# Optimization experiments

Hardware: AMD Instinct MI355X
Metric: run time of the kernel (lower is better)

## Reference

```python
import jax, jax.numpy as jnp
import numpy as np
import math

# BDH config (defaults from BDHConfig)
D = 256        # n_embd
NH = 4         # n_head
MULT = 128     # mlp_internal_dim_multiplier
N = MULT * D // NH   # 8192 latent dim per head
NLAYER = 6
VOCAB = 256
B, T = 1, 1024
THETA = 2.0 ** 16
TWO_PI = 2.0 * math.pi


def _freqs(n):
    # get_freqs: quantize exponent to even integers
    t = jnp.arange(n, dtype=jnp.float32)
    q = jnp.floor(t / 2.0) * 2.0
    return 1.0 / (THETA ** (q / n)) / TWO_PI  # [N]


def _ln(x, eps=1e-5):
    # LayerNorm without affine params (elementwise_affine=False)
    m = jnp.mean(x, axis=-1, keepdims=True)
    v = jnp.mean((x - m) ** 2, axis=-1, keepdims=True)
    return (x - m) / jnp.sqrt(v + eps)


def _rope(phases, v):
    # phases: [T,N] broadcastable to v [...,T,N]
    ph = (phases % 1.0) * TWO_PI
    cos, sin = jnp.cos(ph), jnp.sin(ph)
    # rotate adjacent pairs: (-v_odd, v_even) interleaved
    vrot = jnp.stack((-v[..., 1::2], v[..., ::2]), axis=-1).reshape(v.shape)
    return v * cos + vrot * sin


def setup_inputs() -> dict:
    key = jax.random.key(0)
    ks = jax.random.split(key, 6)
    std = 0.02
    return {
        "idx": jax.random.randint(ks[0], (B, T), 0, VOCAB),
        "embed_w": jax.random.normal(ks[1], (VOCAB, D), jnp.float32) * std,
        "encoder": jax.random.normal(ks[2], (NH, D, N), jnp.float32) * std,
        "encoder_v": jax.random.normal(ks[3], (NH, D, N), jnp.float32) * std,
        "decoder": jax.random.normal(ks[4], (NH * N, D), jnp.float32) * std,
        "lm_head": jax.random.normal(ks[5], (D, VOCAB), jnp.float32) * std,
    }


def reference(idx, embed_w, encoder, encoder_v, decoder, lm_head):
    freqs = _freqs(N)                                             # [N]
    phases = jnp.arange(T, dtype=jnp.float32)[:, None] * freqs    # [T,N]
    mask = jnp.tril(jnp.ones((T, T), jnp.float32), k=-1)          # strict causal
    dec = decoder.reshape(NH, N, D)

    x = _ln(embed_w[idx])                                         # [B,T,D]
    for _ in range(NLAYER):
        x_sp = jax.nn.relu(jnp.einsum('btd,hdn->bhtn', x, encoder))   # [B,nh,T,N]
        qr = _rope(phases, x_sp)                                       # [B,nh,T,N]
        scores = jnp.einsum('bhtn,bhsn->bhts', qr, qr) * mask          # [B,nh,T,T]
        ykv = _ln(jnp.einsum('bhts,bsd->bhtd', scores, x))             # [B,nh,T,D]
        y_sp = jax.nn.relu(jnp.einsum('bhtd,hdn->bhtn', ykv, encoder_v))
        xy = x_sp * y_sp                                               # [B,nh,T,N]
        ymlp = jnp.einsum('bhtn,hnd->btd', xy, dec)                    # [B,T,D]
        x = _ln(x + _ln(ymlp))
    return x @ lm_head                                                 # [B,T,VOCAB]
```

## Files before the change

kernel.cpp:

```cpp
#include <hip/hip_runtime.h>
#include <hip/hip_bf16.h>
#include <math.h>

#define T_ 1024
#define D_ 256
#define N_ 8192
#define NH_ 4
#define NLAYER_ 6
#define VOCAB_ 256
#define TWO_PI_F 6.283185307179586f
#define INV_TWO_PI_F 0.15915494309189535f

#define SC_HSTR32 294912u
#define SC_SSTR32 1179648u
#define SC_SPLIT_BYTES 4718592u
#define SC_NSPLIT 8

typedef __attribute__((ext_vector_type(8))) short short8;
typedef __attribute__((ext_vector_type(4))) float floatx4;
typedef unsigned short ushort_t;

__device__ __forceinline__ void cp16(const void* g, void* l) {
    __builtin_amdgcn_global_load_lds((const __attribute__((address_space(1))) unsigned int*)g,
                                     (__attribute__((address_space(3))) unsigned int*)l,
                                     16, 0, 0);
}

__device__ __forceinline__ float bf2f_raw(unsigned short u) {
    union { unsigned int i; float f; } x;
    x.i = ((unsigned int)u) << 16;
    return x.f;
}
__device__ __forceinline__ unsigned int f2bf_u(float f) {
    union { float f; unsigned int u; } x; x.f = f;
    return (x.u + 0x7fffu + ((x.u >> 16) & 1u)) >> 16;
}

__device__ __forceinline__ float block_sum(float v, float* red) {
    int tid = threadIdx.x;
    red[tid] = v;
    __syncthreads();
    #pragma unroll
    for (int s = 128; s > 0; s >>= 1) {
        if (tid < s) red[tid] += red[tid + s];
        __syncthreads();
    }
    float r = red[0];
    __syncthreads();
    return r;
}


__global__ void k_embed_ln(const int* __restrict__ idx, const float* __restrict__ ew,
                           float* __restrict__ x, __hip_bfloat16* __restrict__ x_bf) {
    __shared__ float red[256];
    int t = blockIdx.x, d = threadIdx.x;
    float v = ew[idx[t] * D_ + d];
    float mean = block_sum(v, red) * (1.0f / D_);
    float c = v - mean;
    float var = block_sum(c * c, red) * (1.0f / D_);
    float o = c * rsqrtf(var + 1e-5f);
    x[t * D_ + d] = o;
    x_bf[t * D_ + d] = __float2bfloat16(o);
}

__global__ void k_ln_rows(const float* __restrict__ yp, __hip_bfloat16* __restrict__ outb) {
    __shared__ float red[256];
    int r = blockIdx.x, d = threadIdx.x;
    const size_t S = (size_t)NH_ * T_ * D_;
    float v = yp[(size_t)r * D_ + d] + yp[S + (size_t)r * D_ + d];
    float mean = block_sum(v, red) * (1.0f / D_);
    float c = v - mean;
    float var = block_sum(c * c, red) * (1.0f / D_);
    outb[(size_t)r * D_ + d] = __float2bfloat16(c * rsqrtf(var + 1e-5f));
}

__global__ void k_x_update(float* __restrict__ x, const float* __restrict__ ypart,
                           __hip_bfloat16* __restrict__ x_bf) {
    __shared__ float red[256];
    int t = blockIdx.x, d = threadIdx.x;
    float v = 0.0f;
    #pragma unroll
    for (int i = 0; i < 32; i++) v += ypart[(size_t)i * T_ * D_ + t * D_ + d];
    float m1 = block_sum(v, red) * (1.0f / D_);
    float c1 = v - m1;
    float v1 = block_sum(c1 * c1, red) * (1.0f / D_);
    float u = c1 * rsqrtf(v1 + 1e-5f);
    float w = x[t * D_ + d] + u;
    float m2 = block_sum(w, red) * (1.0f / D_);
    float c2 = w - m2;
    float v2 = block_sum(c2 * c2, red) * (1.0f / D_);
    float o = c2 * rsqrtf(v2 + 1e-5f);
    x[t * D_ + d] = o;
    x_bf[t * D_ + d] = __float2bfloat16(o);
}

__global__ __launch_bounds__(256) void k_tcvt(const float* __restrict__ in,
                                              __hip_bfloat16* __restrict__ out,
                                              int R, int C) {
    int h = blockIdx.z;
    int r0 = blockIdx.y * 32, c0 = blockIdx.x * 32;
    __shared__ float tile[32][33];
    int tx = threadIdx.x & 31, ty = threadIdx.x >> 5;
    const float* inh = in + (size_t)h * R * C;
    __hip_bfloat16* outh = out + (size_t)h * R * C;
    #pragma unroll
    for (int i = 0; i < 4; i++)
        tile[ty + 8 * i][tx] = inh[(size_t)(r0 + ty + 8 * i) * C + c0 + tx];
    __syncthreads();
    #pragma unroll
    for (int i = 0; i < 4; i++)
        outh[(size_t)(c0 + ty + 8 * i) * R + r0 + tx] = __float2bfloat16(tile[tx][ty + 8 * i]);
}

__device__ __forceinline__ void gemm128(const ushort_t* __restrict__ A,
                                        const ushort_t* __restrict__ B,
                                        int lda, int ldb, int K,
                                        ushort_t* As, ushort_t* Bs,
                                        floatx4 acc[4][4]) {
    const int tid = threadIdx.x;
    const int lane = tid & 63, wid = tid >> 6;
    const int wm = wid >> 1, wn = wid & 1;
    const int quad = lane >> 4, col = lane & 15;
    int srow[4], scol[4];
    #pragma unroll
    for (int i = 0; i < 4; i++) {
        int s = i * 256 + tid;
        srow[i] = s >> 3;
        scol[i] = (s & 7) ^ (srow[i] & 7);
    }
    for (int k0 = 0; k0 < K; k0 += 64) {
        #pragma unroll
        for (int i = 0; i < 4; i++)
            cp16(A + (size_t)srow[i] * lda + k0 + scol[i] * 8,
                 As + (size_t)(i * 256 + wid * 64) * 8);
        #pragma unroll
        for (int i = 0; i < 4; i++)
            cp16(B + (size_t)srow[i] * ldb + k0 + scol[i] * 8,
                 Bs + (size_t)(i * 256 + wid * 64) * 8);
        __syncthreads();
        #pragma unroll
        for (int kk = 0; kk < 2; kk++) {
            short8 af[4], bf[4];
            #pragma unroll
            for (int mi = 0; mi < 4; mi++) {
                int row = wm * 64 + mi * 16 + col;
                int pc = ((kk << 2) + quad) ^ (row & 7);
                af[mi] = *(const short8*)&As[row * 64 + pc * 8];
            }
            #pragma unroll
            for (int ni = 0; ni < 4; ni++) {
                int row = wn * 64 + ni * 16 + col;
                int pc = ((kk << 2) + quad) ^ (row & 7);
                bf[ni] = *(const short8*)&Bs[row * 64 + pc * 8];
            }
            #pragma unroll
            for (int mi = 0; mi < 4; mi++)
                #pragma unroll
                for (int ni = 0; ni < 4; ni++)
                    acc[mi][ni] = __builtin_amdgcn_mfma_f32_16x16x32_bf16(
                        af[mi], bf[ni], acc[mi][ni], 0, 0, 0);
        }
        __syncthreads();
    }
}

#define GEMM_PROLOGUE()                                              \
    __shared__ __align__(16) ushort_t As[128 * 64];                  \
    __shared__ __align__(16) ushort_t Bs[128 * 64];                  \
    floatx4 acc[4][4];                                               \
    _Pragma("unroll") for (int mi = 0; mi < 4; mi++)                 \
        _Pragma("unroll") for (int ni = 0; ni < 4; ni++)             \
            acc[mi][ni] = (floatx4){0.f, 0.f, 0.f, 0.f};             \
    const int lane = threadIdx.x & 63, wid = threadIdx.x >> 6;       \
    const int wm = wid >> 1, wn = wid & 1;                           \
    const int quad = lane >> 4, col = lane & 15;                     \
    const int odd = lane & 1;                                        \
    const int rsel = odd ? 2 : 0, rother = odd ? 0 : 2;

__global__ __launch_bounds__(256) void k_scores_m(const __hip_bfloat16* __restrict__ qr,
                                                  __hip_bfloat16* __restrict__ scp) {
    const int b = blockIdx.x;
    const int slice = b & 31;
    const int h = slice & 3, ks = slice >> 2;
    int i = b >> 5;
    int ti = 0;
    while ((ti + 1) * (ti + 2) / 2 <= i) ti++;
    int si = i - ti * (ti + 1) / 2;
    const int t0 = ti * 128, s0 = si * 128;
    GEMM_PROLOGUE();
    const ushort_t* qh = (const ushort_t*)qr + (size_t)h * T_ * N_ + (size_t)ks * (N_ / 8);
    gemm128(qh + (size_t)t0 * N_, qh + (size_t)s0 * N_, N_, N_, N_ / 8, As, Bs, acc);
    const int W = (ti + 1) * 128;
    unsigned int* sch = (unsigned int*)scp + (size_t)ks * SC_SSTR32 + (size_t)h * SC_HSTR32
                        + (size_t)4096 * ti * (ti + 1);
    #pragma unroll
    for (int mi = 0; mi < 4; mi++)
        #pragma unroll
        for (int ni = 0; ni < 4; ni++) {
            const int ss = s0 + wn * 64 + ni * 16 + col;
            const int ss_e = ss & ~1;
            const int rowb = wm * 64 + mi * 16 + quad * 4;
            #pragma unroll
            for (int rr = 0; rr < 2; rr++) {
                int tt_o = rowb + rother + rr;
                float send = (ss < t0 + tt_o) ? acc[mi][ni][rother + rr] : 0.0f;
                float recv = __shfl_xor(send, 1);
                int tt = rowb + rsel + rr;
                float mine = (ss < t0 + tt) ? acc[mi][ni][rsel + rr] : 0.0f;
                float lo = odd ? recv : mine, hi = odd ? mine : recv;
                sch[((size_t)tt * W + ss_e) >> 1] = f2bf_u(lo) | (f2bf_u(hi) << 16);
            }
        }
}

__global__ void k_sc_cvt(__hip_bfloat16* __restrict__ scp) {
    unsigned int* sp = (unsigned int*)scp;
    unsigned int idx = blockIdx.x * 256 + threadIdx.x;
    #pragma unroll
    for (int r = 0; r < 4; r++) {
        size_t off = (size_t)idx + (size_t)r * SC_HSTR32;
        float lo = 0.f, hi = 0.f;
        #pragma unroll
        for (int s = 0; s < SC_NSPLIT; s++) {
            unsigned int w = sp[off + (size_t)s * SC_SSTR32];
            lo += bf2f_raw((unsigned short)(w & 0xffff));
            hi += bf2f_raw((unsigned short)(w >> 16));
        }
        sp[off] = f2bf_u(lo) | (f2bf_u(hi) << 16);
    }
}

template <int MODE>
__global__ __launch_bounds__(256) void k_proj_m(const __hip_bfloat16* __restrict__ Abf,
                                                const __hip_bfloat16* __restrict__ Wt,
                                                __hip_bfloat16* __restrict__ out1) {
    const int h = blockIdx.z;
    const int t0 = blockIdx.y * 128, n0 = blockIdx.x * 128;
    GEMM_PROLOGUE();
    const ushort_t* Ah = (const ushort_t*)Abf + (MODE ? (size_t)h * T_ * D_ : (size_t)0)
                         + (size_t)t0 * D_;
    const ushort_t* Bh = (const ushort_t*)Wt + (size_t)h * N_ * D_ + (size_t)n0 * D_;
    gemm128(Ah, Bh, D_, D_, D_, As, Bs, acc);
    unsigned int* o1 = (unsigned int*)out1;
    #pragma unroll
    for (int ni = 0; ni < 4; ni++) {
        const int nn_e = (n0 + wn * 64 + ni * 16 + col) & ~1;
        const float freq = exp2f((float)(nn_e >> 1) * (-1.0f / 256.0f)) * INV_TWO_PI_F;
        #pragma unroll
        for (int mi = 0; mi < 4; mi++) {
            const int rowb = t0 + wm * 64 + mi * 16 + quad * 4;
            #pragma unroll
            for (int rr = 0; rr < 2; rr++) {
                float send = fmaxf(acc[mi][ni][rother + rr], 0.0f);
                float recv = __shfl_xor(send, 1);
                float mine = fmaxf(acc[mi][ni][rsel + rr], 0.0f);
                float ve = odd ? recv : mine, vo = odd ? mine : recv;
                int tt = rowb + rsel + rr;
                size_t o32 = (((size_t)h * T_ + tt) * (size_t)N_ + nn_e) >> 1;
                float ph = (float)tt * freq;
                ph -= floorf(ph);
                float s, c;
                __sincosf(ph * TWO_PI_F, &s, &c);
                if (MODE == 0) {
                    o1[o32] = f2bf_u(ve * c - vo * s) | (f2bf_u(vo * c + ve * s) << 16);
                } else {
                    unsigned int xw = o1[o32];
                    float qe = bf2f_raw((unsigned short)(xw & 0xffff));
                    float qo = bf2f_raw((unsigned short)(xw >> 16));
                    float xe = qe * c + qo * s;
                    float xo = qo * c - qe * s;
                    o1[o32] = f2bf_u(ve * xe) | (f2bf_u(vo * xo) << 16);
                }
            }
        }
    }
}

__global__ __launch_bounds__(256) void k_ykv_m(const __hip_bfloat16* __restrict__ sc,
                                               const __hip_bfloat16* __restrict__ xT,
                                               float* __restrict__ ykvp) {
    const int b = blockIdx.x;
    const int h = (b >> 1) & 3, ks = b & 1;
    const int r0 = b >> 3;
    const int d0 = (r0 & 1) * 128, t0 = (r0 >> 1) * 128;
    GEMM_PROLOGUE();
    const int W = t0 + 128;
    const int half = W >> 1;
    const int ti = t0 >> 7;
    const ushort_t* Ah = (const ushort_t*)sc + (size_t)h * 589824u
                         + (size_t)8192 * ti * (ti + 1) + (size_t)ks * half;
    const ushort_t* Bh = (const ushort_t*)xT + (size_t)d0 * T_ + (size_t)ks * half;
    gemm128(Ah, Bh, W, T_, half, As, Bs, acc);
    float2* yp = (float2*)(ykvp + (size_t)ks * NH_ * T_ * D_);
    #pragma unroll
    for (int mi = 0; mi < 4; mi++)
        #pragma unroll
        for (int ni = 0; ni < 4; ni++) {
            const int dd_e = (d0 + wn * 64 + ni * 16 + col) & ~1;
            const int rowb = t0 + wm * 64 + mi * 16 + quad * 4;
            #pragma unroll
            for (int rr = 0; rr < 2; rr++) {
                float send = acc[mi][ni][rother + rr];
                float recv = __shfl_xor(send, 1);
                float mine = acc[mi][ni][rsel + rr];
                int tt = rowb + rsel + rr;
                yp[(((size_t)h * T_ + tt) * D_ + dd_e) >> 1] =
                    odd ? make_float2(recv, mine) : make_float2(mine, recv);
            }
        }
}

__global__ __launch_bounds__(256) void k_ymlp_m(const __hip_bfloat16* __restrict__ xy,
                                                const __hip_bfloat16* __restrict__ decT,
                                                float* __restrict__ ypart) {
    const int b = blockIdx.x;
    const int slice = b & 31;
    const int ks = slice >> 2, h = slice & 3;
    const int r0 = b >> 5;
    const int d0 = (r0 & 1) * 128, t0 = (r0 >> 1) * 128;
    GEMM_PROLOGUE();
    const ushort_t* Ah = (const ushort_t*)xy + (size_t)h * T_ * N_ + (size_t)t0 * N_ + ks * 1024;
    const ushort_t* Bh = (const ushort_t*)decT + (size_t)h * D_ * N_ + (size_t)d0 * N_ + ks * 1024;
    gemm128(Ah, Bh, N_, N_, 1024, As, Bs, acc);
    float2* yp = (float2*)(ypart + (size_t)slice * T_ * D_);
    #pragma unroll
    for (int mi = 0; mi < 4; mi++)
        #pragma unroll
        for (int ni = 0; ni < 4; ni++) {
            const int dd_e = (d0 + wn * 64 + ni * 16 + col) & ~1;
            const int rowb = t0 + wm * 64 + mi * 16 + quad * 4;
            #pragma unroll
            for (int rr = 0; rr < 2; rr++) {
                float send = acc[mi][ni][rother + rr];
                float recv = __shfl_xor(send, 1);
                float mine = acc[mi][ni][rsel + rr];
                int tt = rowb + rsel + rr;
                yp[((size_t)tt * D_ + dd_e) >> 1] =
                    odd ? make_float2(recv, mine) : make_float2(mine, recv);
            }
        }
}

__global__ __launch_bounds__(256) void k_lmhead_m(const __hip_bfloat16* __restrict__ x_bf,
                                                  const __hip_bfloat16* __restrict__ lmT,
                                                  float* __restrict__ out) {
    const int v0 = blockIdx.x * 128, t0 = blockIdx.y * 128;
    GEMM_PROLOGUE();
    const ushort_t* Ah = (const ushort_t*)x_bf + (size_t)t0 * D_;
    const ushort_t* Bh = (const ushort_t*)lmT + (size_t)v0 * D_;
    gemm128(Ah, Bh, D_, D_, D_, As, Bs, acc);
    float2* op = (float2*)out;
    #pragma unroll
    for (int mi = 0; mi < 4; mi++)
        #pragma unroll
        for (int ni = 0; ni < 4; ni++) {
            const int vv_e = (v0 + wn * 64 + ni * 16 + col) & ~1;
            const int rowb = t0 + wm * 64 + mi * 16 + quad * 4;
            #pragma unroll
            for (int rr = 0; rr < 2; rr++) {
                float send = acc[mi][ni][rother + rr];
                float recv = __shfl_xor(send, 1);
                float mine = acc[mi][ni][rsel + rr];
                int tt = rowb + rsel + rr;
                op[((size_t)tt * VOCAB_ + vv_e) >> 1] =
                    odd ? make_float2(recv, mine) : make_float2(mine, recv);
            }
        }
}


extern "C" void kernel_launch(void* const* d_in, const int* in_sizes, int n_in,
                              void* d_out, int out_size, void* d_ws, size_t ws_size,
                              hipStream_t stream) {
    const int* idx = (const int*)d_in[0];
    const float* embed_w = (const float*)d_in[1];
    const float* encoder = (const float*)d_in[2];
    const float* encoder_v = (const float*)d_in[3];
    const float* decoder = (const float*)d_in[4];
    const float* lm_head = (const float*)d_in[5];
    float* out = (float*)d_out;

    char* p = (char*)d_ws;
    auto alloc = [&](size_t bytes) {
        char* q = p;
        p += (bytes + 255) & ~(size_t)255;
        return q;
    };
    float* x = (float*)alloc((size_t)T_ * D_ * 4);
    __hip_bfloat16* x_bf = (__hip_bfloat16*)alloc((size_t)T_ * D_ * 2);
    __hip_bfloat16* xT = (__hip_bfloat16*)alloc((size_t)T_ * D_ * 2);
    __hip_bfloat16* ykv_bf = (__hip_bfloat16*)alloc((size_t)NH_ * T_ * D_ * 2);
    __hip_bfloat16* scp = (__hip_bfloat16*)alloc((size_t)SC_NSPLIT * SC_SPLIT_BYTES);
    __hip_bfloat16* qr = (__hip_bfloat16*)alloc((size_t)NH_ * T_ * N_ * 2);
    __hip_bfloat16* encT = (__hip_bfloat16*)alloc((size_t)NH_ * N_ * D_ * 2);
    __hip_bfloat16* encvT = (__hip_bfloat16*)alloc((size_t)NH_ * N_ * D_ * 2);
    __hip_bfloat16* decT = (__hip_bfloat16*)alloc((size_t)NH_ * N_ * D_ * 2);
    __hip_bfloat16* lmT = (__hip_bfloat16*)alloc((size_t)VOCAB_ * D_ * 2);
    float* ypart = (float*)alloc((size_t)32 * T_ * D_ * 4);
    float* ykvp = (float*)((char*)scp + SC_SPLIT_BYTES);

    k_tcvt<<<dim3(N_ / 32, D_ / 32, NH_), 256, 0, stream>>>(encoder, encT, D_, N_);
    k_tcvt<<<dim3(N_ / 32, D_ / 32, NH_), 256, 0, stream>>>(encoder_v, encvT, D_, N_);
    k_tcvt<<<dim3(D_ / 32, N_ / 32, NH_), 256, 0, stream>>>(decoder, decT, N_, D_);
    k_tcvt<<<dim3(VOCAB_ / 32, D_ / 32, 1), 256, 0, stream>>>(lm_head, lmT, D_, VOCAB_);

    k_embed_ln<<<T_, 256, 0, stream>>>(idx, embed_w, x, x_bf);
    for (int l = 0; l < NLAYER_; l++) {
        k_proj_m<0><<<dim3(N_ / 128, T_ / 128, NH_), 256, 0, stream>>>(x_bf, encT, qr);
        k_scores_m<<<36 * 32, 256, 0, stream>>>(qr, scp);
        k_sc_cvt<<<1152, 256, 0, stream>>>(scp);
        k_tcvt<<<dim3(D_ / 32, T_ / 32, 1), 256, 0, stream>>>(x, xT, T_, D_);
        k_ykv_m<<<16 * 8, 256, 0, stream>>>(scp, xT, ykvp);
        k_ln_rows<<<NH_ * T_, 256, 0, stream>>>(ykvp, ykv_bf);
        k_proj_m<1><<<dim3(N_ / 128, T_ / 128, NH_), 256, 0, stream>>>(ykv_bf, encvT, qr );
        k_ymlp_m<<<16 * 32, 256, 0, stream>>>(qr, decT, ypart);
        k_x_update<<<T_, 256, 0, stream>>>(x, ypart, x_bf);
    }
    k_lmhead_m<<<dim3(VOCAB_ / 128, T_ / 128), 256, 0, stream>>>(x_bf, lmT, out);
}
```

Before: 1.348 ms.

## Double-buffer GEMM LDS tiles, batch epilogue loads, use native sin/cos

The shared 128x128 GEMM mainloop now uses two LDS buffers, so the next K-tile is issued with global_load_lds while the current tile feeds the MFMAs, with one barrier per step instead of two. The MODE 1 projection epilogue loads all previous xw words up front to overlap their latency, and __sincosf is replaced with the hardware v_sin/v_cos instructions, which take phase in revolutions. In exchange, LDS use doubles, which may lower occupancy, and more values stay live in registers.

```diff
diff --git a/kernel.cpp b/kernel.cpp
--- a/kernel.cpp
+++ b/kernel.cpp
@@ -15,6 +15,7 @@
 #define SC_SSTR32 1179648u
 #define SC_SPLIT_BYTES 4718592u
 #define SC_NSPLIT 8
+#define TILE_E (128 * 64)
 
 typedef __attribute__((ext_vector_type(8))) short short8;
 typedef __attribute__((ext_vector_type(4))) float floatx4;
@@ -34,6 +35,12 @@
 __device__ __forceinline__ unsigned int f2bf_u(float f) {
     union { float f; unsigned int u; } x; x.f = f;
     return (x.u + 0x7fffu + ((x.u >> 16) & 1u)) >> 16;
+}
+__device__ __forceinline__ float fsin_rev(float ph) {
+    float r; asm("v_sin_f32 %0, %1" : "=v"(r) : "v"(ph)); return r;
+}
+__device__ __forceinline__ float fcos_rev(float ph) {
+    float r; asm("v_cos_f32 %0, %1" : "=v"(r) : "v"(ph)); return r;
 }
 
 __device__ __forceinline__ float block_sum(float v, float* red) {
@@ -113,13 +120,56 @@
         outh[(size_t)(c0 + ty + 8 * i) * R + r0 + tx] = __float2bfloat16(tile[tx][ty + 8 * i]);
 }
 
+
+__device__ __forceinline__ void stage_tile(const ushort_t* __restrict__ A,
+                                           const ushort_t* __restrict__ B,
+                                           int lda, int ldb, int k0,
+                                           ushort_t* As, ushort_t* Bs,
+                                           const int* srow, const int* scol, int wid) {
+    #pragma unroll
+    for (int i = 0; i < 4; i++)
+        cp16(A + (size_t)srow[i] * lda + k0 + scol[i] * 8,
+             As + (size_t)(i * 256 + wid * 64) * 8);
+    #pragma unroll
+    for (int i = 0; i < 4; i++)
+        cp16(B + (size_t)srow[i] * ldb + k0 + scol[i] * 8,
+             Bs + (size_t)(i * 256 + wid * 64) * 8);
+}
+
+__device__ __forceinline__ void compute_tile(const ushort_t* As, const ushort_t* Bs,
+                                             floatx4 acc[4][4],
+                                             int wm, int wn, int quad, int col) {
+    #pragma unroll
+    for (int kk = 0; kk < 2; kk++) {
+        short8 af[4], bf[4];
+        #pragma unroll
+        for (int mi = 0; mi < 4; mi++) {
+            int row = wm * 64 + mi * 16 + col;
+            int pc = ((kk << 2) + quad) ^ (row & 7);
+            af[mi] = *(const short8*)&As[row * 64 + pc * 8];
+        }
+        #pragma unroll
+        for (int ni = 0; ni < 4; ni++) {
+            int row = wn * 64 + ni * 16 + col;
+            int pc = ((kk << 2) + quad) ^ (row & 7);
+            bf[ni] = *(const short8*)&Bs[row * 64 + pc * 8];
+        }
+        #pragma unroll
+        for (int mi = 0; mi < 4; mi++)
+            #pragma unroll
+            for (int ni = 0; ni < 4; ni++)
+                acc[mi][ni] = __builtin_amdgcn_mfma_f32_16x16x32_bf16(
+                    af[mi], bf[ni], acc[mi][ni], 0, 0, 0);
+    }
+}
+
 __device__ __forceinline__ void gemm128(const ushort_t* __restrict__ A,
                                         const ushort_t* __restrict__ B,
                                         int lda, int ldb, int K,
                                         ushort_t* As, ushort_t* Bs,
                                         floatx4 acc[4][4]) {
     const int tid = threadIdx.x;
-    const int lane = tid & 63, wid = tid >> 6;
+    const int wid = tid >> 6, lane = tid & 63;
     const int wm = wid >> 1, wn = wid & 1;
     const int quad = lane >> 4, col = lane & 15;
     int srow[4], scol[4];
@@ -129,45 +179,24 @@
         srow[i] = s >> 3;
         scol[i] = (s & 7) ^ (srow[i] & 7);
     }
-    for (int k0 = 0; k0 < K; k0 += 64) {
-        #pragma unroll
-        for (int i = 0; i < 4; i++)
-            cp16(A + (size_t)srow[i] * lda + k0 + scol[i] * 8,
-                 As + (size_t)(i * 256 + wid * 64) * 8);
-        #pragma unroll
-        for (int i = 0; i < 4; i++)
-            cp16(B + (size_t)srow[i] * ldb + k0 + scol[i] * 8,
-                 Bs + (size_t)(i * 256 + wid * 64) * 8);
-        __syncthreads();
-        #pragma unroll
-        for (int kk = 0; kk < 2; kk++) {
-            short8 af[4], bf[4];
-            #pragma unroll
-            for (int mi = 0; mi < 4; mi++) {
-                int row = wm * 64 + mi * 16 + col;
-                int pc = ((kk << 2) + quad) ^ (row & 7);
-                af[mi] = *(const short8*)&As[row * 64 + pc * 8];
-            }
-            #pragma unroll
-            for (int ni = 0; ni < 4; ni++) {
-                int row = wn * 64 + ni * 16 + col;
-                int pc = ((kk << 2) + quad) ^ (row & 7);
-                bf[ni] = *(const short8*)&Bs[row * 64 + pc * 8];
-            }
-            #pragma unroll
-            for (int mi = 0; mi < 4; mi++)
-                #pragma unroll
-                for (int ni = 0; ni < 4; ni++)
-                    acc[mi][ni] = __builtin_amdgcn_mfma_f32_16x16x32_bf16(
-                        af[mi], bf[ni], acc[mi][ni], 0, 0, 0);
-        }
-        __syncthreads();
+    const int nt = K >> 6;
+    stage_tile(A, B, lda, ldb, 0, As, Bs, srow, scol, wid);
+    asm volatile("s_waitcnt vmcnt(0)" ::: "memory");
+    asm volatile("s_barrier" ::: "memory");
+    for (int t = 0; t < nt; ++t) {
+        const int cur = t & 1;
+        if (t + 1 < nt)
+            stage_tile(A, B, lda, ldb, (t + 1) * 64,
+                       As + (cur ^ 1) * TILE_E, Bs + (cur ^ 1) * TILE_E, srow, scol, wid);
+        compute_tile(As + cur * TILE_E, Bs + cur * TILE_E, acc, wm, wn, quad, col);
+        asm volatile("s_waitcnt vmcnt(0)" ::: "memory");
+        asm volatile("s_barrier" ::: "memory");
     }
 }
 
 #define GEMM_PROLOGUE()                                              \
-    __shared__ __align__(16) ushort_t As[128 * 64];                  \
-    __shared__ __align__(16) ushort_t Bs[128 * 64];                  \
+    __shared__ __align__(16) ushort_t As[2 * TILE_E];                \
+    __shared__ __align__(16) ushort_t Bs[2 * TILE_E];                \
     floatx4 acc[4][4];                                               \
     _Pragma("unroll") for (int mi = 0; mi < 4; mi++)                 \
         _Pragma("unroll") for (int ni = 0; ni < 4; ni++)             \
@@ -243,6 +272,22 @@
     const ushort_t* Bh = (const ushort_t*)Wt + (size_t)h * N_ * D_ + (size_t)n0 * D_;
     gemm128(Ah, Bh, D_, D_, D_, As, Bs, acc);
     unsigned int* o1 = (unsigned int*)out1;
+    unsigned int xw[4][4][2];
+    if (MODE == 1) {
+        #pragma unroll
+        for (int ni = 0; ni < 4; ni++) {
+            const int nn_e = (n0 + wn * 64 + ni * 16 + col) & ~1;
+            #pragma unroll
+            for (int mi = 0; mi < 4; mi++) {
+                const int rowb = t0 + wm * 64 + mi * 16 + quad * 4;
+                #pragma unroll
+                for (int rr = 0; rr < 2; rr++) {
+                    int tt = rowb + rsel + rr;
+                    xw[ni][mi][rr] = o1[(((size_t)h * T_ + tt) * (size_t)N_ + nn_e) >> 1];
+                }
+            }
+        }
+    }
     #pragma unroll
     for (int ni = 0; ni < 4; ni++) {
         const int nn_e = (n0 + wn * 64 + ni * 16 + col) & ~1;
@@ -260,14 +305,13 @@
                 size_t o32 = (((size_t)h * T_ + tt) * (size_t)N_ + nn_e) >> 1;
                 float ph = (float)tt * freq;
                 ph -= floorf(ph);
-                float s, c;
-                __sincosf(ph * TWO_PI_F, &s, &c);
+                float c = fcos_rev(ph), s = fsin_rev(ph);
                 if (MODE == 0) {
                     o1[o32] = f2bf_u(ve * c - vo * s) | (f2bf_u(vo * c + ve * s) << 16);
                 } else {
-                    unsigned int xw = o1[o32];
-                    float qe = bf2f_raw((unsigned short)(xw & 0xffff));
-                    float qo = bf2f_raw((unsigned short)(xw >> 16));
+                    unsigned int w = xw[ni][mi][rr];
+                    float qe = bf2f_raw((unsigned short)(w & 0xffff));
+                    float qo = bf2f_raw((unsigned short)(w >> 16));
                     float xe = qe * c + qo * s;
                     float xo = qo * c - qe * s;
                     o1[o32] = f2bf_u(ve * xe) | (f2bf_u(vo * xo) << 16);
```

Result: slower. 1.464 ms (+8.6%).
